# Kernel tuning notes

Measured on AMD Instinct MI355X. Metric: run time of the kernel, lower is better.

Reference implementation:

```python
import jax, jax.numpy as jnp
import numpy as np

BS, V, N, C_IN, C_OUT = 8, 4096, 16, 64, 64


def setup_inputs() -> dict:
    key = jax.random.key(0)
    k1, k2, k3, k4, k5 = jax.random.split(key, 5)
    stdv = 1.0 / np.sqrt(N * C_IN)
    return {
        "neighbor_index": jax.random.randint(k1, (BS, V, N), 0, V, dtype=jnp.int64),
        "vertices": jax.random.normal(k2, (BS, V, 3), dtype=jnp.float32),
        "feature_map": jax.random.normal(k3, (BS, V, C_IN), dtype=jnp.float32),
        "weights": jax.random.uniform(k4, (C_OUT, (N + 1) * C_IN), dtype=jnp.float32, minval=-stdv, maxval=stdv),
        "bias": jax.random.uniform(k5, (C_OUT,), dtype=jnp.float32, minval=-stdv, maxval=stdv),
    }


def reference(neighbor_index, vertices, feature_map, weights, bias):
    bs, v, n = neighbor_index.shape
    # gather neighbor features per batch element: (bs, v, n, c)
    neighbors = jax.vmap(lambda f, idx: f[idx])(feature_map, neighbor_index)
    # prepend self feature: (bs, v, n+1, c)
    feats = jnp.concatenate([feature_map[:, :, None, :], neighbors], axis=2)
    # torch permutes to (bs, c, n+1, v) then reshapes -> flat index = c*(n+1)+k,
    # equivalent to transposing last two dims here before flattening
    flat = feats.transpose(0, 1, 3, 2).reshape(bs, v, -1)  # (bs, v, c*(n+1))
    out = jnp.einsum('bvf,of->bvo', flat, weights) + bias
    return jax.nn.relu(out)
```

## Files before the change

kernel.cpp:

```cpp
#include <hip/hip_runtime.h>
#include <stdint.h>

#define NV 4096

typedef __attribute__((ext_vector_type(8))) short bf16x8;
typedef __attribute__((ext_vector_type(4))) float f32x4;

__device__ __forceinline__ unsigned short f2bf(float f) {
  union { float f; unsigned int u; } v; v.f = f;
  unsigned int r = v.u + 0x7FFF + ((v.u >> 16) & 1);
  return (unsigned short)(r >> 16);
}

__global__ __launch_bounds__(256)
void prep(const float* __restrict__ fm, const float* __restrict__ w,
          unsigned short* __restrict__ fmb, unsigned short* __restrict__ wb) {
  int blk = blockIdx.x;
  if (blk < 1024) {
    int i = (blk * 256 + threadIdx.x) * 8;
    float4 v0 = *(const float4*)(fm + i);
    float4 v1 = *(const float4*)(fm + i + 4);
    ushort4 o0, o1;
    o0.x = f2bf(v0.x); o0.y = f2bf(v0.y); o0.z = f2bf(v0.z); o0.w = f2bf(v0.w);
    o1.x = f2bf(v1.x); o1.y = f2bf(v1.y); o1.z = f2bf(v1.z); o1.w = f2bf(v1.w);
    *(ushort4*)(fmb + i) = o0;
    *(ushort4*)(fmb + i + 4) = o1;
  } else {
    int t = (blk - 1024) * 256 + threadIdx.x;
    int c = t & 63;
    int o = (t >> 6) & 63;
    int k = t >> 12;
    wb[t] = f2bf(w[o * 1088 + c * 17 + k]);
  }
}

__global__ __launch_bounds__(256, 2)
void conv_main(const int* __restrict__ nbr, const unsigned short* __restrict__ fmb,
               const unsigned short* __restrict__ wb, const float* __restrict__ bias,
               float* __restrict__ out) {
  __shared__ unsigned char smem[49152];

  const int bid = blockIdx.x;
  const int b = bid & 7;
  const int tile = bid >> 3;
  const int tid = threadIdx.x;
  const int lane = tid & 63;
  const int lm = lane & 15;
  const int lk = lane >> 4;
  const int w4 = tid >> 6;
  const int rg = w4 >> 1;
  const int h = w4 & 1;

  const int rbase = tile * 64;
  const bf16x8* fb8 = (const bf16x8*)(fmb + (size_t)b * NV * 64);

  const int r0 = tid >> 3;
  const int c8 = tid & 7;
  const int swz = c8 ^ (r0 & 7);
  const int row0g = rbase + r0;
  const int row1g = rbase + r0 + 32;

  const int4* q0 = (const int4*)(nbr + ((size_t)b * NV + row0g) * 16);
  const int4* q1 = (const int4*)(nbr + ((size_t)b * NV + row1g) * 16);
  const int4 i0a = q0[0], i0b = q0[1], i0c = q0[2], i0d = q0[3];
  const int4 i1a = q1[0], i1b = q1[1], i1c = q1[2], i1d = q1[3];

  const int fsl = h * 4 + lk;
  const int offW = lm * 128 + ((fsl ^ (lm & 7)) << 4);
  const int rowL0 = rg * 32 + lm;
  const int rowL1 = rg * 32 + 16 + lm;
  const int offA0 = rowL0 * 128 + ((fsl ^ (rowL0 & 7)) << 4);
  const int offA1 = rowL1 * 128 + ((fsl ^ (rowL1 & 7)) << 4);

  f32x4 accA0{0,0,0,0}, accA1{0,0,0,0}, accA2{0,0,0,0}, accA3{0,0,0,0};
  f32x4 accB0{0,0,0,0}, accB1{0,0,0,0}, accB2{0,0,0,0}, accB3{0,0,0,0};

#define SBR __builtin_amdgcn_sched_barrier(0)
#define MFMA __builtin_amdgcn_mfma_f32_16x16x32_bf16

#define STAGE(SLOT, BUF, SVA, SVB) {                                        \
    _Pragma("unroll")                                                       \
    for (int i_ = 0; i_ < 2; ++i_) {                                        \
      int t_ = i_ * 256 + tid;                                              \
      int o_ = t_ >> 3, s_ = t_ & 7;                                        \
      const unsigned short* ws_ =                                           \
          wb + (SLOT) * 4096 + o_ * 64 + ((s_ ^ (o_ & 7)) << 3);            \
      __builtin_amdgcn_global_load_lds(                                     \
          (const __attribute__((address_space(1))) void*)ws_,               \
          (__attribute__((address_space(3))) void*)(smem + (BUF) * 8192 + t_ * 16), \
          16, 0, 0);                                                        \
    }                                                                       \
    {                                                                       \
      const bf16x8* fa_ = fb8 + (size_t)(SVA) * 8 + swz;                    \
      __builtin_amdgcn_global_load_lds(                                     \
          (const __attribute__((address_space(1))) void*)fa_,               \
          (__attribute__((address_space(3))) void*)(smem + 24576 + (BUF) * 8192 + tid * 16), \
          16, 0, 0);                                                        \
      const bf16x8* fbp_ = fb8 + (size_t)(SVB) * 8 + swz;                   \
      __builtin_amdgcn_global_load_lds(                                     \
          (const __attribute__((address_space(1))) void*)fbp_,              \
          (__attribute__((address_space(3))) void*)(smem + 24576 + (BUF) * 8192 + 4096 + tid * 16), \
          16, 0, 0);                                                        \
    }                                                                       \
  }

#define CONSUME(BUF) {                                                     \
    const char* wp_ = (const char*)smem + (BUF) * 8192;                    \
    const char* fp_ = (const char*)smem + 24576 + (BUF) * 8192;            \
    bf16x8 W0 = *(const bf16x8*)(wp_ + 0 * 2048 + offW);                   \
    bf16x8 W1 = *(const bf16x8*)(wp_ + 1 * 2048 + offW);                   \
    bf16x8 W2 = *(const bf16x8*)(wp_ + 2 * 2048 + offW);                   \
    bf16x8 W3 = *(const bf16x8*)(wp_ + 3 * 2048 + offW);                   \
    bf16x8 A0 = *(const bf16x8*)(fp_ + offA0);                             \
    bf16x8 A1 = *(const bf16x8*)(fp_ + offA1);                             \
    accA0 = MFMA(A0, W0, accA0, 0, 0, 0);                                  \
    accA1 = MFMA(A0, W1, accA1, 0, 0, 0);                                  \
    accA2 = MFMA(A0, W2, accA2, 0, 0, 0);                                  \
    accA3 = MFMA(A0, W3, accA3, 0, 0, 0);                                  \
    accB0 = MFMA(A1, W0, accB0, 0, 0, 0);                                  \
    accB1 = MFMA(A1, W1, accB1, 0, 0, 0);                                  \
    accB2 = MFMA(A1, W2, accB2, 0, 0, 0);                                  \
    accB3 = MFMA(A1, W3, accB3, 0, 0, 0);                                  \
  }

#define WAITBAR(N)                                                          \
    SBR; asm volatile("s_waitcnt vmcnt(" #N ")" ::: "memory"); SBR;         \
    __builtin_amdgcn_s_barrier(); SBR;

  STAGE(0, 0, row0g, row1g); SBR;
  STAGE(1, 1, i0a.x, i1a.x); SBR;
  WAITBAR(4);

  STAGE(2, 2, i0a.y, i1a.y);  SBR; CONSUME(0); WAITBAR(4);
  STAGE(3, 0, i0a.z, i1a.z);  SBR; CONSUME(1); WAITBAR(4);
  STAGE(4, 1, i0a.w, i1a.w);  SBR; CONSUME(2); WAITBAR(4);
  STAGE(5, 2, i0b.x, i1b.x);  SBR; CONSUME(0); WAITBAR(4);
  STAGE(6, 0, i0b.y, i1b.y);  SBR; CONSUME(1); WAITBAR(4);
  STAGE(7, 1, i0b.z, i1b.z);  SBR; CONSUME(2); WAITBAR(4);
  STAGE(8, 2, i0b.w, i1b.w);  SBR; CONSUME(0); WAITBAR(4);
  STAGE(9, 0, i0c.x, i1c.x);  SBR; CONSUME(1); WAITBAR(4);
  STAGE(10, 1, i0c.y, i1c.y); SBR; CONSUME(2); WAITBAR(4);
  STAGE(11, 2, i0c.z, i1c.z); SBR; CONSUME(0); WAITBAR(4);
  STAGE(12, 0, i0c.w, i1c.w); SBR; CONSUME(1); WAITBAR(4);
  STAGE(13, 1, i0d.x, i1d.x); SBR; CONSUME(2); WAITBAR(4);
  STAGE(14, 2, i0d.y, i1d.y); SBR; CONSUME(0); WAITBAR(4);
  STAGE(15, 0, i0d.z, i1d.z); SBR; CONSUME(1); WAITBAR(4);
  STAGE(16, 1, i0d.w, i1d.w); SBR; CONSUME(2); WAITBAR(4);
  CONSUME(0); WAITBAR(0);
  CONSUME(1);

#undef WAITBAR
#undef CONSUME
#undef STAGE
#undef MFMA
#undef SBR

  __syncthreads();
  if (h == 1) {
    float* rp = (float*)smem + rg * 2048 + lane * 4;
    *(f32x4*)(rp + 0 * 256) = accA0;
    *(f32x4*)(rp + 1 * 256) = accA1;
    *(f32x4*)(rp + 2 * 256) = accA2;
    *(f32x4*)(rp + 3 * 256) = accA3;
    *(f32x4*)(rp + 4 * 256) = accB0;
    *(f32x4*)(rp + 5 * 256) = accB1;
    *(f32x4*)(rp + 6 * 256) = accB2;
    *(f32x4*)(rp + 7 * 256) = accB3;
  }
  __syncthreads();
  if (h == 0) {
    const float* rp = (const float*)smem + rg * 2048 + lane * 4;
    accA0 += *(const f32x4*)(rp + 0 * 256);
    accA1 += *(const f32x4*)(rp + 1 * 256);
    accA2 += *(const f32x4*)(rp + 2 * 256);
    accA3 += *(const f32x4*)(rp + 3 * 256);
    accB0 += *(const f32x4*)(rp + 4 * 256);
    accB1 += *(const f32x4*)(rp + 5 * 256);
    accB2 += *(const f32x4*)(rp + 6 * 256);
    accB3 += *(const f32x4*)(rp + 7 * 256);

    const float bv0 = bias[lm];
    const float bv1 = bias[16 + lm];
    const float bv2 = bias[32 + lm];
    const float bv3 = bias[48 + lm];
    float* op = out + (size_t)b * NV * 64;
    #pragma unroll
    for (int mt = 0; mt < 2; ++mt) {
      const int gv = rbase + rg * 32 + mt * 16 + lk * 4;
      #pragma unroll
      for (int r = 0; r < 4; ++r) {
        float* orow = op + (size_t)(gv + r) * 64;
        if (mt == 0) {
          orow[lm]      = fmaxf(accA0[r] + bv0, 0.f);
          orow[16 + lm] = fmaxf(accA1[r] + bv1, 0.f);
          orow[32 + lm] = fmaxf(accA2[r] + bv2, 0.f);
          orow[48 + lm] = fmaxf(accA3[r] + bv3, 0.f);
        } else {
          orow[lm]      = fmaxf(accB0[r] + bv0, 0.f);
          orow[16 + lm] = fmaxf(accB1[r] + bv1, 0.f);
          orow[32 + lm] = fmaxf(accB2[r] + bv2, 0.f);
          orow[48 + lm] = fmaxf(accB3[r] + bv3, 0.f);
        }
      }
    }
  }
}

extern "C" void kernel_launch(void* const* d_in, const int* in_sizes, int n_in,
                              void* d_out, int out_size, void* d_ws, size_t ws_size,
                              hipStream_t stream) {
  const int* nbr = (const int*)d_in[0];
  const float* fm = (const float*)d_in[2];
  const float* w = (const float*)d_in[3];
  const float* bias = (const float*)d_in[4];
  float* out = (float*)d_out;

  unsigned short* fmb = (unsigned short*)d_ws;
  unsigned short* wb = fmb + (size_t)8 * NV * 64;

  prep<<<1296, 256, 0, stream>>>(fm, w, fmb, wb);
  conv_main<<<512, 256, 0, stream>>>(nbr, fmb, wb, bias, out);
}
```

Measured before the change: 19.88 us.

## Preload all weights into LDS and give each wave a private gather pipeline

After: 23.01 us. 1.16x slower.

```diff
diff --git a/kernel.cpp b/kernel.cpp
--- a/kernel.cpp
+++ b/kernel.cpp
@@ -34,11 +34,11 @@
   }
 }
 
-__global__ __launch_bounds__(256, 2)
+__global__ __launch_bounds__(256, 1)
 void conv_main(const int* __restrict__ nbr, const unsigned short* __restrict__ fmb,
                const unsigned short* __restrict__ wb, const float* __restrict__ bias,
                float* __restrict__ out) {
-  __shared__ unsigned char smem[49152];
+  extern __shared__ unsigned char smem[];
 
   const int bid = blockIdx.x;
   const int b = bid & 7;
@@ -54,104 +54,133 @@
   const int rbase = tile * 64;
   const bf16x8* fb8 = (const bf16x8*)(fmb + (size_t)b * NV * 64);
 
-  const int r0 = tid >> 3;
-  const int c8 = tid & 7;
-  const int swz = c8 ^ (r0 & 7);
-  const int row0g = rbase + r0;
-  const int row1g = rbase + r0 + 32;
-
-  const int4* q0 = (const int4*)(nbr + ((size_t)b * NV + row0g) * 16);
-  const int4* q1 = (const int4*)(nbr + ((size_t)b * NV + row1g) * 16);
-  const int4 i0a = q0[0], i0b = q0[1], i0c = q0[2], i0d = q0[3];
-  const int4 i1a = q1[0], i1b = q1[1], i1c = q1[2], i1d = q1[3];
+  const int grA = rbase + rg * 32 + (lane >> 2);
+  const int grB = grA + 16;
+  const int gsrc = h * 4 + ((lane & 3) ^ ((lane >> 3) & 3));
+
+  const int4* qA = (const int4*)(nbr + ((size_t)b * NV + grA) * 16);
+  const int4* qB = (const int4*)(nbr + ((size_t)b * NV + grB) * 16);
+  const int4 iAa = qA[0], iAb = qA[1], iAc = qA[2], iAd = qA[3];
+  const int4 iBa = qB[0], iBb = qB[1], iBc = qB[2], iBd = qB[3];
 
   const int fsl = h * 4 + lk;
+  const bf16x8* w16p = (const bf16x8*)(wb + 16 * 4096);
+  const bf16x8 X0 = w16p[(0 * 16 + lm) * 8 + fsl];
+  const bf16x8 X1 = w16p[(1 * 16 + lm) * 8 + fsl];
+  const bf16x8 X2 = w16p[(2 * 16 + lm) * 8 + fsl];
+  const bf16x8 X3 = w16p[(3 * 16 + lm) * 8 + fsl];
+
+#define SBR __builtin_amdgcn_sched_barrier(0)
+#define MFMA __builtin_amdgcn_mfma_f32_16x16x32_bf16
+
+  #pragma unroll
+  for (int i = 0; i < 32; ++i) {
+    int t = i * 256 + tid;
+    int o = (t >> 3) & 63;
+    int s8 = t & 7;
+    int seg = s8 ^ (o & 7);
+    const unsigned short* src = wb + (size_t)(t >> 9) * 4096 + o * 64 + seg * 8;
+    __builtin_amdgcn_global_load_lds(
+        (const __attribute__((address_space(1))) void*)src,
+        (__attribute__((address_space(3))) void*)(smem + (size_t)t * 16), 16, 0, 0);
+  }
+  SBR;
+
+  unsigned char* fbase = smem + 131072 + w4 * 6144;
+
+#define STAGE_F(SA, SB, C) {                                                 \
+    const bf16x8* sa_ = fb8 + (size_t)(SA) * 8 + gsrc;                       \
+    __builtin_amdgcn_global_load_lds(                                        \
+        (const __attribute__((address_space(1))) void*)sa_,                  \
+        (__attribute__((address_space(3))) void*)(fbase + (C) * 2048 + lane * 16), \
+        16, 0, 0);                                                           \
+    const bf16x8* sb_ = fb8 + (size_t)(SB) * 8 + gsrc;                       \
+    __builtin_amdgcn_global_load_lds(                                        \
+        (const __attribute__((address_space(1))) void*)sb_,                  \
+        (__attribute__((address_space(3))) void*)(fbase + (C) * 2048 + 1024 + lane * 16), \
+        16, 0, 0);                                                           \
+  }
+
+  STAGE_F(grA, grB, 0); SBR;
+  STAGE_F(iAa.x, iBa.x, 1); SBR;
+  STAGE_F(iAa.y, iBa.y, 2); SBR;
+  asm volatile("s_waitcnt vmcnt(6)" ::: "memory"); SBR;
+  __syncthreads();
+
+  const int offA0 = lm * 64 + ((lk ^ ((lm >> 1) & 3)) << 4);
   const int offW = lm * 128 + ((fsl ^ (lm & 7)) << 4);
-  const int rowL0 = rg * 32 + lm;
-  const int rowL1 = rg * 32 + 16 + lm;
-  const int offA0 = rowL0 * 128 + ((fsl ^ (rowL0 & 7)) << 4);
-  const int offA1 = rowL1 * 128 + ((fsl ^ (rowL1 & 7)) << 4);
 
   f32x4 accA0{0,0,0,0}, accA1{0,0,0,0}, accA2{0,0,0,0}, accA3{0,0,0,0};
   f32x4 accB0{0,0,0,0}, accB1{0,0,0,0}, accB2{0,0,0,0}, accB3{0,0,0,0};
 
-#define SBR __builtin_amdgcn_sched_barrier(0)
-#define MFMA __builtin_amdgcn_mfma_f32_16x16x32_bf16
-
-#define STAGE(SLOT, BUF, SVA, SVB) {                                        \
-    _Pragma("unroll")                                                       \
-    for (int i_ = 0; i_ < 2; ++i_) {                                        \
-      int t_ = i_ * 256 + tid;                                              \
-      int o_ = t_ >> 3, s_ = t_ & 7;                                        \
-      const unsigned short* ws_ =                                           \
-          wb + (SLOT) * 4096 + o_ * 64 + ((s_ ^ (o_ & 7)) << 3);            \
-      __builtin_amdgcn_global_load_lds(                                     \
-          (const __attribute__((address_space(1))) void*)ws_,               \
-          (__attribute__((address_space(3))) void*)(smem + (BUF) * 8192 + t_ * 16), \
-          16, 0, 0);                                                        \
-    }                                                                       \
-    {                                                                       \
-      const bf16x8* fa_ = fb8 + (size_t)(SVA) * 8 + swz;                    \
-      __builtin_amdgcn_global_load_lds(                                     \
-          (const __attribute__((address_space(1))) void*)fa_,               \
-          (__attribute__((address_space(3))) void*)(smem + 24576 + (BUF) * 8192 + tid * 16), \
-          16, 0, 0);                                                        \
-      const bf16x8* fbp_ = fb8 + (size_t)(SVB) * 8 + swz;                   \
-      __builtin_amdgcn_global_load_lds(                                     \
-          (const __attribute__((address_space(1))) void*)fbp_,              \
-          (__attribute__((address_space(3))) void*)(smem + 24576 + (BUF) * 8192 + 4096 + tid * 16), \
-          16, 0, 0);                                                        \
-    }                                                                       \
-  }
-
-#define CONSUME(BUF) {                                                     \
-    const char* wp_ = (const char*)smem + (BUF) * 8192;                    \
-    const char* fp_ = (const char*)smem + 24576 + (BUF) * 8192;            \
-    bf16x8 W0 = *(const bf16x8*)(wp_ + 0 * 2048 + offW);                   \
-    bf16x8 W1 = *(const bf16x8*)(wp_ + 1 * 2048 + offW);                   \
-    bf16x8 W2 = *(const bf16x8*)(wp_ + 2 * 2048 + offW);                   \
-    bf16x8 W3 = *(const bf16x8*)(wp_ + 3 * 2048 + offW);                   \
-    bf16x8 A0 = *(const bf16x8*)(fp_ + offA0);                             \
-    bf16x8 A1 = *(const bf16x8*)(fp_ + offA1);                             \
-    accA0 = MFMA(A0, W0, accA0, 0, 0, 0);                                  \
-    accA1 = MFMA(A0, W1, accA1, 0, 0, 0);                                  \
-    accA2 = MFMA(A0, W2, accA2, 0, 0, 0);                                  \
-    accA3 = MFMA(A0, W3, accA3, 0, 0, 0);                                  \
-    accB0 = MFMA(A1, W0, accB0, 0, 0, 0);                                  \
-    accB1 = MFMA(A1, W1, accB1, 0, 0, 0);                                  \
-    accB2 = MFMA(A1, W2, accB2, 0, 0, 0);                                  \
-    accB3 = MFMA(A1, W3, accB3, 0, 0, 0);                                  \
-  }
-
-#define WAITBAR(N)                                                          \
-    SBR; asm volatile("s_waitcnt vmcnt(" #N ")" ::: "memory"); SBR;         \
-    __builtin_amdgcn_s_barrier(); SBR;
-
-  STAGE(0, 0, row0g, row1g); SBR;
-  STAGE(1, 1, i0a.x, i1a.x); SBR;
-  WAITBAR(4);
-
-  STAGE(2, 2, i0a.y, i1a.y);  SBR; CONSUME(0); WAITBAR(4);
-  STAGE(3, 0, i0a.z, i1a.z);  SBR; CONSUME(1); WAITBAR(4);
-  STAGE(4, 1, i0a.w, i1a.w);  SBR; CONSUME(2); WAITBAR(4);
-  STAGE(5, 2, i0b.x, i1b.x);  SBR; CONSUME(0); WAITBAR(4);
-  STAGE(6, 0, i0b.y, i1b.y);  SBR; CONSUME(1); WAITBAR(4);
-  STAGE(7, 1, i0b.z, i1b.z);  SBR; CONSUME(2); WAITBAR(4);
-  STAGE(8, 2, i0b.w, i1b.w);  SBR; CONSUME(0); WAITBAR(4);
-  STAGE(9, 0, i0c.x, i1c.x);  SBR; CONSUME(1); WAITBAR(4);
-  STAGE(10, 1, i0c.y, i1c.y); SBR; CONSUME(2); WAITBAR(4);
-  STAGE(11, 2, i0c.z, i1c.z); SBR; CONSUME(0); WAITBAR(4);
-  STAGE(12, 0, i0c.w, i1c.w); SBR; CONSUME(1); WAITBAR(4);
-  STAGE(13, 1, i0d.x, i1d.x); SBR; CONSUME(2); WAITBAR(4);
-  STAGE(14, 2, i0d.y, i1d.y); SBR; CONSUME(0); WAITBAR(4);
-  STAGE(15, 0, i0d.z, i1d.z); SBR; CONSUME(1); WAITBAR(4);
-  STAGE(16, 1, i0d.w, i1d.w); SBR; CONSUME(2); WAITBAR(4);
-  CONSUME(0); WAITBAR(0);
-  CONSUME(1);
-
-#undef WAITBAR
-#undef CONSUME
-#undef STAGE
+#define MFMAS(W0_, W1_, W2_, W3_)                                  \
+    accA0 = MFMA(A0, W0_, accA0, 0, 0, 0);                         \
+    accA1 = MFMA(A0, W1_, accA1, 0, 0, 0);                         \
+    accA2 = MFMA(A0, W2_, accA2, 0, 0, 0);                         \
+    accA3 = MFMA(A0, W3_, accA3, 0, 0, 0);                         \
+    accB0 = MFMA(A1, W0_, accB0, 0, 0, 0);                         \
+    accB1 = MFMA(A1, W1_, accB1, 0, 0, 0);                         \
+    accB2 = MFMA(A1, W2_, accB2, 0, 0, 0);                         \
+    accB3 = MFMA(A1, W3_, accB3, 0, 0, 0);
+
+#define STEP(K, CNT, SAN, SBN)                                               \
+  asm volatile("s_waitcnt vmcnt(" #CNT ")" ::: "memory"); SBR;               \
+  {                                                                          \
+    const unsigned char* fp_ = fbase + ((K) % 3) * 2048;                     \
+    bf16x8 A0 = *(const bf16x8*)(fp_ + offA0);                               \
+    bf16x8 A1 = *(const bf16x8*)(fp_ + 1024 + offA0);                        \
+    const unsigned char* wp_ = smem + (K) * 8192;                            \
+    bf16x8 W0 = *(const bf16x8*)(wp_ + offW);                                \
+    bf16x8 W1 = *(const bf16x8*)(wp_ + 2048 + offW);                         \
+    bf16x8 W2 = *(const bf16x8*)(wp_ + 4096 + offW);                         \
+    bf16x8 W3 = *(const bf16x8*)(wp_ + 6144 + offW);                         \
+    asm volatile("s_waitcnt lgkmcnt(0)" ::: "memory"); SBR;                  \
+    STAGE_F(SAN, SBN, (K) % 3); SBR;                                         \
+    MFMAS(W0, W1, W2, W3)                                                    \
+  }
+
+#define STEPN(K, CNT)                                                        \
+  asm volatile("s_waitcnt vmcnt(" #CNT ")" ::: "memory"); SBR;               \
+  {                                                                          \
+    const unsigned char* fp_ = fbase + ((K) % 3) * 2048;                     \
+    bf16x8 A0 = *(const bf16x8*)(fp_ + offA0);                               \
+    bf16x8 A1 = *(const bf16x8*)(fp_ + 1024 + offA0);                        \
+    const unsigned char* wp_ = smem + (K) * 8192;                            \
+    bf16x8 W0 = *(const bf16x8*)(wp_ + offW);                                \
+    bf16x8 W1 = *(const bf16x8*)(wp_ + 2048 + offW);                         \
+    bf16x8 W2 = *(const bf16x8*)(wp_ + 4096 + offW);                         \
+    bf16x8 W3 = *(const bf16x8*)(wp_ + 6144 + offW);                         \
+    MFMAS(W0, W1, W2, W3)                                                    \
+  }
+
+  STEP(0, 4, iAa.z, iBa.z)
+  STEP(1, 4, iAa.w, iBa.w)
+  STEP(2, 4, iAb.x, iBb.x)
+  STEP(3, 4, iAb.y, iBb.y)
+  STEP(4, 4, iAb.z, iBb.z)
+  STEP(5, 4, iAb.w, iBb.w)
+  STEP(6, 4, iAc.x, iBc.x)
+  STEP(7, 4, iAc.y, iBc.y)
+  STEP(8, 4, iAc.z, iBc.z)
+  STEP(9, 4, iAc.w, iBc.w)
+  STEP(10, 4, iAd.x, iBd.x)
+  STEP(11, 4, iAd.y, iBd.y)
+  STEP(12, 4, iAd.z, iBd.z)
+  STEP(13, 4, iAd.w, iBd.w)
+  STEPN(14, 4)
+  STEPN(15, 2)
+  asm volatile("s_waitcnt vmcnt(0)" ::: "memory"); SBR;
+  {
+    const unsigned char* fp_ = fbase + 1 * 2048;
+    bf16x8 A0 = *(const bf16x8*)(fp_ + offA0);
+    bf16x8 A1 = *(const bf16x8*)(fp_ + 1024 + offA0);
+    MFMAS(X0, X1, X2, X3)
+  }
+
+#undef STEPN
+#undef STEP
+#undef MFMAS
+#undef STAGE_F
 #undef MFMA
 #undef SBR
 
@@ -218,6 +247,9 @@
   unsigned short* fmb = (unsigned short*)d_ws;
   unsigned short* wb = fmb + (size_t)8 * NV * 64;
 
+  hipFuncSetAttribute((const void*)conv_main,
+                      hipFuncAttributeMaxDynamicSharedMemorySize, 155648);
+
   prep<<<1296, 256, 0, stream>>>(fm, w, fmb, wb);
-  conv_main<<<512, 256, 0, stream>>>(nbr, fmb, wb, bias, out);
-}
+  conv_main<<<512, 256, 155648, stream>>>(nbr, fmb, wb, bias, out);
+}
```

## Gather fp32 features directly and convert to bf16 in the main kernel

Applied to the files above, without the earlier changes.

Result: slower. 21.99 us (+10.6%).

```diff
diff --git a/kernel.cpp b/kernel.cpp
--- a/kernel.cpp
+++ b/kernel.cpp
@@ -1,4 +1,5 @@
 #include <hip/hip_runtime.h>
+#include <hip/hip_bf16.h>
 #include <stdint.h>
 
 #define NV 4096
@@ -13,32 +14,28 @@
 }
 
 __global__ __launch_bounds__(256)
-void prep(const float* __restrict__ fm, const float* __restrict__ w,
-          unsigned short* __restrict__ fmb, unsigned short* __restrict__ wb) {
-  int blk = blockIdx.x;
-  if (blk < 1024) {
-    int i = (blk * 256 + threadIdx.x) * 8;
-    float4 v0 = *(const float4*)(fm + i);
-    float4 v1 = *(const float4*)(fm + i + 4);
-    ushort4 o0, o1;
-    o0.x = f2bf(v0.x); o0.y = f2bf(v0.y); o0.z = f2bf(v0.z); o0.w = f2bf(v0.w);
-    o1.x = f2bf(v1.x); o1.y = f2bf(v1.y); o1.z = f2bf(v1.z); o1.w = f2bf(v1.w);
-    *(ushort4*)(fmb + i) = o0;
-    *(ushort4*)(fmb + i + 4) = o1;
-  } else {
-    int t = (blk - 1024) * 256 + threadIdx.x;
-    int c = t & 63;
-    int o = (t >> 6) & 63;
-    int k = t >> 12;
-    wb[t] = f2bf(w[o * 1088 + c * 17 + k]);
-  }
+void prep_w(const float* __restrict__ w, unsigned short* __restrict__ wb) {
+  int t = blockIdx.x * 256 + threadIdx.x;
+  int c = t & 63;
+  int o = (t >> 6) & 63;
+  int k = t >> 12;
+  wb[t] = f2bf(w[o * 1088 + c * 17 + k]);
+}
+
+__device__ __forceinline__ bf16x8 cvt8(f32x4 lo, f32x4 hi) {
+  union { bf16x8 v; __hip_bfloat162 h[4]; } u;
+  u.h[0] = __float22bfloat162_rn(make_float2(lo[0], lo[1]));
+  u.h[1] = __float22bfloat162_rn(make_float2(lo[2], lo[3]));
+  u.h[2] = __float22bfloat162_rn(make_float2(hi[0], hi[1]));
+  u.h[3] = __float22bfloat162_rn(make_float2(hi[2], hi[3]));
+  return u.v;
 }
 
 __global__ __launch_bounds__(256, 2)
-void conv_main(const int* __restrict__ nbr, const unsigned short* __restrict__ fmb,
+void conv_main(const int* __restrict__ nbr, const float* __restrict__ fm,
                const unsigned short* __restrict__ wb, const float* __restrict__ bias,
                float* __restrict__ out) {
-  __shared__ unsigned char smem[49152];
+  __shared__ unsigned char smem[77824];
 
   const int bid = blockIdx.x;
   const int b = bid & 7;
@@ -52,25 +49,11 @@
   const int h = w4 & 1;
 
   const int rbase = tile * 64;
-  const bf16x8* fb8 = (const bf16x8*)(fmb + (size_t)b * NV * 64);
-
-  const int r0 = tid >> 3;
-  const int c8 = tid & 7;
-  const int swz = c8 ^ (r0 & 7);
-  const int row0g = rbase + r0;
-  const int row1g = rbase + r0 + 32;
-
-  const int4* q0 = (const int4*)(nbr + ((size_t)b * NV + row0g) * 16);
-  const int4* q1 = (const int4*)(nbr + ((size_t)b * NV + row1g) * 16);
-  const int4 i0a = q0[0], i0b = q0[1], i0c = q0[2], i0d = q0[3];
-  const int4 i1a = q1[0], i1b = q1[1], i1c = q1[2], i1d = q1[3];
+  const float* fb32 = fm + (size_t)b * NV * 64;
 
   const int fsl = h * 4 + lk;
   const int offW = lm * 128 + ((fsl ^ (lm & 7)) << 4);
-  const int rowL0 = rg * 32 + lm;
-  const int rowL1 = rg * 32 + 16 + lm;
-  const int offA0 = rowL0 * 128 + ((fsl ^ (rowL0 & 7)) << 4);
-  const int offA1 = rowL1 * 128 + ((fsl ^ (rowL1 & 7)) << 4);
+  const int offF0 = (rg * 32 + lm) * 256 + (((2 * fsl) ^ ((lm & 7) << 1)) << 4);
 
   f32x4 accA0{0,0,0,0}, accA1{0,0,0,0}, accA2{0,0,0,0}, accA3{0,0,0,0};
   f32x4 accB0{0,0,0,0}, accB1{0,0,0,0}, accB2{0,0,0,0}, accB3{0,0,0,0};
@@ -78,41 +61,47 @@
 #define SBR __builtin_amdgcn_sched_barrier(0)
 #define MFMA __builtin_amdgcn_mfma_f32_16x16x32_bf16
 
-#define STAGE(SLOT, BUF, SVA, SVB) {                                        \
+#define STAGE(K, C) {                                                       \
     _Pragma("unroll")                                                       \
     for (int i_ = 0; i_ < 2; ++i_) {                                        \
       int t_ = i_ * 256 + tid;                                              \
-      int o_ = t_ >> 3, s_ = t_ & 7;                                        \
+      int o_ = (t_ >> 3) & 63, s_ = t_ & 7;                                 \
       const unsigned short* ws_ =                                           \
-          wb + (SLOT) * 4096 + o_ * 64 + ((s_ ^ (o_ & 7)) << 3);            \
+          wb + (K) * 4096 + o_ * 64 + ((s_ ^ (o_ & 7)) << 3);               \
       __builtin_amdgcn_global_load_lds(                                     \
           (const __attribute__((address_space(1))) void*)ws_,               \
-          (__attribute__((address_space(3))) void*)(smem + (BUF) * 8192 + t_ * 16), \
+          (__attribute__((address_space(3))) void*)(smem + (C) * 8192 + t_ * 16), \
           16, 0, 0);                                                        \
     }                                                                       \
-    {                                                                       \
-      const bf16x8* fa_ = fb8 + (size_t)(SVA) * 8 + swz;                    \
+    _Pragma("unroll")                                                       \
+    for (int i_ = 0; i_ < 4; ++i_) {                                        \
+      int row_ = w4 * 16 + i_ * 4 + (lane >> 4);                            \
+      int sv_;                                                              \
+      if ((K) == 0) sv_ = rbase + row_;                                     \
+      else sv_ = *(const int*)(smem + 73728 + row_ * 64 + ((K) - 1) * 4);   \
+      int gs_ = (lane & 15) ^ ((row_ & 7) << 1);                            \
+      const float* fs_ = fb32 + (size_t)sv_ * 64 + gs_ * 4;                 \
       __builtin_amdgcn_global_load_lds(                                     \
-          (const __attribute__((address_space(1))) void*)fa_,               \
-          (__attribute__((address_space(3))) void*)(smem + 24576 + (BUF) * 8192 + tid * 16), \
-          16, 0, 0);                                                        \
-      const bf16x8* fbp_ = fb8 + (size_t)(SVB) * 8 + swz;                   \
-      __builtin_amdgcn_global_load_lds(                                     \
-          (const __attribute__((address_space(1))) void*)fbp_,              \
-          (__attribute__((address_space(3))) void*)(smem + 24576 + (BUF) * 8192 + 4096 + tid * 16), \
+          (const __attribute__((address_space(1))) void*)fs_,               \
+          (__attribute__((address_space(3))) void*)(smem + 24576 + (C) * 16384 \
+              + (size_t)row_ * 256 + (lane & 15) * 16),                     \
           16, 0, 0);                                                        \
     }                                                                       \
   }
 
-#define CONSUME(BUF) {                                                     \
-    const char* wp_ = (const char*)smem + (BUF) * 8192;                    \
-    const char* fp_ = (const char*)smem + 24576 + (BUF) * 8192;            \
+#define CONSUME(K, C) {                                                    \
+    const unsigned char* wp_ = smem + (C) * 8192;                          \
+    const unsigned char* fp_ = smem + 24576 + (C) * 16384;                 \
     bf16x8 W0 = *(const bf16x8*)(wp_ + 0 * 2048 + offW);                   \
     bf16x8 W1 = *(const bf16x8*)(wp_ + 1 * 2048 + offW);                   \
     bf16x8 W2 = *(const bf16x8*)(wp_ + 2 * 2048 + offW);                   \
     bf16x8 W3 = *(const bf16x8*)(wp_ + 3 * 2048 + offW);                   \
-    bf16x8 A0 = *(const bf16x8*)(fp_ + offA0);                             \
-    bf16x8 A1 = *(const bf16x8*)(fp_ + offA1);                             \
+    f32x4 lo0 = *(const f32x4*)(fp_ + offF0);                              \
+    f32x4 hi0 = *(const f32x4*)(fp_ + offF0 + 16);                         \
+    f32x4 lo1 = *(const f32x4*)(fp_ + offF0 + 4096);                       \
+    f32x4 hi1 = *(const f32x4*)(fp_ + offF0 + 4096 + 16);                  \
+    bf16x8 A0 = cvt8(lo0, hi0);                                            \
+    bf16x8 A1 = cvt8(lo1, hi1);                                            \
     accA0 = MFMA(A0, W0, accA0, 0, 0, 0);                                  \
     accA1 = MFMA(A0, W1, accA1, 0, 0, 0);                                  \
     accA2 = MFMA(A0, W2, accA2, 0, 0, 0);                                  \
@@ -127,27 +116,29 @@
     SBR; asm volatile("s_waitcnt vmcnt(" #N ")" ::: "memory"); SBR;         \
     __builtin_amdgcn_s_barrier(); SBR;
 
-  STAGE(0, 0, row0g, row1g); SBR;
-  STAGE(1, 1, i0a.x, i1a.x); SBR;
-  WAITBAR(4);
-
-  STAGE(2, 2, i0a.y, i1a.y);  SBR; CONSUME(0); WAITBAR(4);
-  STAGE(3, 0, i0a.z, i1a.z);  SBR; CONSUME(1); WAITBAR(4);
-  STAGE(4, 1, i0a.w, i1a.w);  SBR; CONSUME(2); WAITBAR(4);
-  STAGE(5, 2, i0b.x, i1b.x);  SBR; CONSUME(0); WAITBAR(4);
-  STAGE(6, 0, i0b.y, i1b.y);  SBR; CONSUME(1); WAITBAR(4);
-  STAGE(7, 1, i0b.z, i1b.z);  SBR; CONSUME(2); WAITBAR(4);
-  STAGE(8, 2, i0b.w, i1b.w);  SBR; CONSUME(0); WAITBAR(4);
-  STAGE(9, 0, i0c.x, i1c.x);  SBR; CONSUME(1); WAITBAR(4);
-  STAGE(10, 1, i0c.y, i1c.y); SBR; CONSUME(2); WAITBAR(4);
-  STAGE(11, 2, i0c.z, i1c.z); SBR; CONSUME(0); WAITBAR(4);
-  STAGE(12, 0, i0c.w, i1c.w); SBR; CONSUME(1); WAITBAR(4);
-  STAGE(13, 1, i0d.x, i1d.x); SBR; CONSUME(2); WAITBAR(4);
-  STAGE(14, 2, i0d.y, i1d.y); SBR; CONSUME(0); WAITBAR(4);
-  STAGE(15, 0, i0d.z, i1d.z); SBR; CONSUME(1); WAITBAR(4);
-  STAGE(16, 1, i0d.w, i1d.w); SBR; CONSUME(2); WAITBAR(4);
-  CONSUME(0); WAITBAR(0);
-  CONSUME(1);
+  const int4 myidx = ((const int4*)(nbr + ((size_t)b * NV + rbase) * 16))[tid];
+  STAGE(0, 0); SBR;
+  ((int4*)(smem + 73728))[tid] = myidx;
+  __syncthreads();
+  STAGE(1, 1); SBR;
+
+  STAGE(2, 2);  SBR; CONSUME(0, 0);  WAITBAR(6);
+  STAGE(3, 0);  SBR; CONSUME(1, 1);  WAITBAR(6);
+  STAGE(4, 1);  SBR; CONSUME(2, 2);  WAITBAR(6);
+  STAGE(5, 2);  SBR; CONSUME(3, 0);  WAITBAR(6);
+  STAGE(6, 0);  SBR; CONSUME(4, 1);  WAITBAR(6);
+  STAGE(7, 1);  SBR; CONSUME(5, 2);  WAITBAR(6);
+  STAGE(8, 2);  SBR; CONSUME(6, 0);  WAITBAR(6);
+  STAGE(9, 0);  SBR; CONSUME(7, 1);  WAITBAR(6);
+  STAGE(10, 1); SBR; CONSUME(8, 2);  WAITBAR(6);
+  STAGE(11, 2); SBR; CONSUME(9, 0);  WAITBAR(6);
+  STAGE(12, 0); SBR; CONSUME(10, 1); WAITBAR(6);
+  STAGE(13, 1); SBR; CONSUME(11, 2); WAITBAR(6);
+  STAGE(14, 2); SBR; CONSUME(12, 0); WAITBAR(6);
+  STAGE(15, 0); SBR; CONSUME(13, 1); WAITBAR(6);
+  STAGE(16, 1); SBR; CONSUME(14, 2); WAITBAR(6);
+  CONSUME(15, 0); WAITBAR(0);
+  CONSUME(16, 1);
 
 #undef WAITBAR
 #undef CONSUME
@@ -215,9 +206,8 @@
   const float* bias = (const float*)d_in[4];
   float* out = (float*)d_out;
 
-  unsigned short* fmb = (unsigned short*)d_ws;
-  unsigned short* wb = fmb + (size_t)8 * NV * 64;
-
-  prep<<<1296, 256, 0, stream>>>(fm, w, fmb, wb);
-  conv_main<<<512, 256, 0, stream>>>(nbr, fmb, wb, bias, out);
-}
+  unsigned short* wb = (unsigned short*)d_ws;
+
+  prep_w<<<272, 256, 0, stream>>>(w, wb);
+  conv_main<<<512, 256, 0, stream>>>(nbr, fm, wb, bias, out);
+}
```

## Split K across four waves with full 64x64 tiles and cross-wave LDS reduction

Applied to the files above, without the earlier changes.

Result: slower. 20.64 us (+3.8%).

```diff
diff --git a/kernel.cpp b/kernel.cpp
--- a/kernel.cpp
+++ b/kernel.cpp
@@ -48,8 +48,8 @@
   const int lm = lane & 15;
   const int lk = lane >> 4;
   const int w4 = tid >> 6;
-  const int rg = w4 >> 1;
-  const int h = w4 & 1;
+  const int p = w4 & 1;
+  const int h = w4 >> 1;
 
   const int rbase = tile * 64;
   const bf16x8* fb8 = (const bf16x8*)(fmb + (size_t)b * NV * 64);
@@ -66,23 +66,21 @@
   const int4 i1a = q1[0], i1b = q1[1], i1c = q1[2], i1d = q1[3];
 
   const int fsl = h * 4 + lk;
-  const int offW = lm * 128 + ((fsl ^ (lm & 7)) << 4);
-  const int rowL0 = rg * 32 + lm;
-  const int rowL1 = rg * 32 + 16 + lm;
-  const int offA0 = rowL0 * 128 + ((fsl ^ (rowL0 & 7)) << 4);
-  const int offA1 = rowL1 * 128 + ((fsl ^ (rowL1 & 7)) << 4);
-
-  f32x4 accA0{0,0,0,0}, accA1{0,0,0,0}, accA2{0,0,0,0}, accA3{0,0,0,0};
-  f32x4 accB0{0,0,0,0}, accB1{0,0,0,0}, accB2{0,0,0,0}, accB3{0,0,0,0};
+  const int offB = lm * 128 + ((fsl ^ (lm & 7)) << 4);
+
+  f32x4 acc00{0,0,0,0}, acc01{0,0,0,0}, acc02{0,0,0,0}, acc03{0,0,0,0};
+  f32x4 acc10{0,0,0,0}, acc11{0,0,0,0}, acc12{0,0,0,0}, acc13{0,0,0,0};
+  f32x4 acc20{0,0,0,0}, acc21{0,0,0,0}, acc22{0,0,0,0}, acc23{0,0,0,0};
+  f32x4 acc30{0,0,0,0}, acc31{0,0,0,0}, acc32{0,0,0,0}, acc33{0,0,0,0};
 
 #define SBR __builtin_amdgcn_sched_barrier(0)
 #define MFMA __builtin_amdgcn_mfma_f32_16x16x32_bf16
 
-#define STAGE(SLOT, BUF, SVA, SVB) {                                        \
+#define STAGE(SLOT, BUF) {                                                  \
     _Pragma("unroll")                                                       \
     for (int i_ = 0; i_ < 2; ++i_) {                                        \
       int t_ = i_ * 256 + tid;                                              \
-      int o_ = t_ >> 3, s_ = t_ & 7;                                        \
+      int o_ = (t_ >> 3) & 63, s_ = t_ & 7;                                 \
       const unsigned short* ws_ =                                           \
           wb + (SLOT) * 4096 + o_ * 64 + ((s_ ^ (o_ & 7)) << 3);            \
       __builtin_amdgcn_global_load_lds(                                     \
@@ -91,119 +89,116 @@
           16, 0, 0);                                                        \
     }                                                                       \
     {                                                                       \
-      const bf16x8* fa_ = fb8 + (size_t)(SVA) * 8 + swz;                    \
+      const bf16x8* fa_ = fb8 + (size_t)(SVA_) * 8 + swz;                   \
       __builtin_amdgcn_global_load_lds(                                     \
           (const __attribute__((address_space(1))) void*)fa_,               \
           (__attribute__((address_space(3))) void*)(smem + 24576 + (BUF) * 8192 + tid * 16), \
           16, 0, 0);                                                        \
-      const bf16x8* fbp_ = fb8 + (size_t)(SVB) * 8 + swz;                   \
+      const bf16x8* fbp_ = fb8 + (size_t)(SVB_) * 8 + swz;                  \
       __builtin_amdgcn_global_load_lds(                                     \
           (const __attribute__((address_space(1))) void*)fbp_,              \
           (__attribute__((address_space(3))) void*)(smem + 24576 + (BUF) * 8192 + 4096 + tid * 16), \
           16, 0, 0);                                                        \
     }                                                                       \
   }
+#define STAGES(SLOT, BUF, SA, SB) { const int SVA_ = (SA), SVB_ = (SB); STAGE(SLOT, BUF) }
 
 #define CONSUME(BUF) {                                                     \
-    const char* wp_ = (const char*)smem + (BUF) * 8192;                    \
-    const char* fp_ = (const char*)smem + 24576 + (BUF) * 8192;            \
-    bf16x8 W0 = *(const bf16x8*)(wp_ + 0 * 2048 + offW);                   \
-    bf16x8 W1 = *(const bf16x8*)(wp_ + 1 * 2048 + offW);                   \
-    bf16x8 W2 = *(const bf16x8*)(wp_ + 2 * 2048 + offW);                   \
-    bf16x8 W3 = *(const bf16x8*)(wp_ + 3 * 2048 + offW);                   \
-    bf16x8 A0 = *(const bf16x8*)(fp_ + offA0);                             \
-    bf16x8 A1 = *(const bf16x8*)(fp_ + offA1);                             \
-    accA0 = MFMA(A0, W0, accA0, 0, 0, 0);                                  \
-    accA1 = MFMA(A0, W1, accA1, 0, 0, 0);                                  \
-    accA2 = MFMA(A0, W2, accA2, 0, 0, 0);                                  \
-    accA3 = MFMA(A0, W3, accA3, 0, 0, 0);                                  \
-    accB0 = MFMA(A1, W0, accB0, 0, 0, 0);                                  \
-    accB1 = MFMA(A1, W1, accB1, 0, 0, 0);                                  \
-    accB2 = MFMA(A1, W2, accB2, 0, 0, 0);                                  \
-    accB3 = MFMA(A1, W3, accB3, 0, 0, 0);                                  \
+    const unsigned char* wp_ = smem + (BUF) * 8192;                        \
+    const unsigned char* fp_ = smem + 24576 + (BUF) * 8192;                \
+    bf16x8 W0 = *(const bf16x8*)(wp_ + offB);                              \
+    bf16x8 W1 = *(const bf16x8*)(wp_ + 2048 + offB);                       \
+    bf16x8 W2 = *(const bf16x8*)(wp_ + 4096 + offB);                       \
+    bf16x8 W3 = *(const bf16x8*)(wp_ + 6144 + offB);                       \
+    bf16x8 A0 = *(const bf16x8*)(fp_ + offB);                              \
+    bf16x8 A1 = *(const bf16x8*)(fp_ + 2048 + offB);                       \
+    bf16x8 A2 = *(const bf16x8*)(fp_ + 4096 + offB);                       \
+    bf16x8 A3 = *(const bf16x8*)(fp_ + 6144 + offB);                       \
+    __builtin_amdgcn_s_setprio(1);                                         \
+    acc00 = MFMA(A0, W0, acc00, 0, 0, 0);                                  \
+    acc01 = MFMA(A0, W1, acc01, 0, 0, 0);                                  \
+    acc02 = MFMA(A0, W2, acc02, 0, 0, 0);                                  \
+    acc03 = MFMA(A0, W3, acc03, 0, 0, 0);                                  \
+    acc10 = MFMA(A1, W0, acc10, 0, 0, 0);                                  \
+    acc11 = MFMA(A1, W1, acc11, 0, 0, 0);                                  \
+    acc12 = MFMA(A1, W2, acc12, 0, 0, 0);                                  \
+    acc13 = MFMA(A1, W3, acc13, 0, 0, 0);                                  \
+    acc20 = MFMA(A2, W0, acc20, 0, 0, 0);                                  \
+    acc21 = MFMA(A2, W1, acc21, 0, 0, 0);                                  \
+    acc22 = MFMA(A2, W2, acc22, 0, 0, 0);                                  \
+    acc23 = MFMA(A2, W3, acc23, 0, 0, 0);                                  \
+    acc30 = MFMA(A3, W0, acc30, 0, 0, 0);                                  \
+    acc31 = MFMA(A3, W1, acc31, 0, 0, 0);                                  \
+    acc32 = MFMA(A3, W2, acc32, 0, 0, 0);                                  \
+    acc33 = MFMA(A3, W3, acc33, 0, 0, 0);                                  \
+    __builtin_amdgcn_s_setprio(0);                                         \
   }
 
 #define WAITBAR(N)                                                          \
     SBR; asm volatile("s_waitcnt vmcnt(" #N ")" ::: "memory"); SBR;         \
     __builtin_amdgcn_s_barrier(); SBR;
 
-  STAGE(0, 0, row0g, row1g); SBR;
-  STAGE(1, 1, i0a.x, i1a.x); SBR;
+  STAGES(0, 0, row0g, row1g); SBR;
+  STAGES(1, 1, i0a.x, i1a.x); SBR;
   WAITBAR(4);
 
-  STAGE(2, 2, i0a.y, i1a.y);  SBR; CONSUME(0); WAITBAR(4);
-  STAGE(3, 0, i0a.z, i1a.z);  SBR; CONSUME(1); WAITBAR(4);
-  STAGE(4, 1, i0a.w, i1a.w);  SBR; CONSUME(2); WAITBAR(4);
-  STAGE(5, 2, i0b.x, i1b.x);  SBR; CONSUME(0); WAITBAR(4);
-  STAGE(6, 0, i0b.y, i1b.y);  SBR; CONSUME(1); WAITBAR(4);
-  STAGE(7, 1, i0b.z, i1b.z);  SBR; CONSUME(2); WAITBAR(4);
-  STAGE(8, 2, i0b.w, i1b.w);  SBR; CONSUME(0); WAITBAR(4);
-  STAGE(9, 0, i0c.x, i1c.x);  SBR; CONSUME(1); WAITBAR(4);
-  STAGE(10, 1, i0c.y, i1c.y); SBR; CONSUME(2); WAITBAR(4);
-  STAGE(11, 2, i0c.z, i1c.z); SBR; CONSUME(0); WAITBAR(4);
-  STAGE(12, 0, i0c.w, i1c.w); SBR; CONSUME(1); WAITBAR(4);
-  STAGE(13, 1, i0d.x, i1d.x); SBR; CONSUME(2); WAITBAR(4);
-  STAGE(14, 2, i0d.y, i1d.y); SBR; CONSUME(0); WAITBAR(4);
-  STAGE(15, 0, i0d.z, i1d.z); SBR; CONSUME(1); WAITBAR(4);
-  STAGE(16, 1, i0d.w, i1d.w); SBR; CONSUME(2); WAITBAR(4);
-  CONSUME(0); WAITBAR(0);
-  CONSUME(1);
+  STAGES(2, 2, i0a.y, i1a.y);  SBR; if (p == 0) CONSUME(0); WAITBAR(4);
+  STAGES(3, 0, i0a.z, i1a.z);  SBR; if (p == 1) CONSUME(1); WAITBAR(4);
+  STAGES(4, 1, i0a.w, i1a.w);  SBR; if (p == 0) CONSUME(2); WAITBAR(4);
+  STAGES(5, 2, i0b.x, i1b.x);  SBR; if (p == 1) CONSUME(0); WAITBAR(4);
+  STAGES(6, 0, i0b.y, i1b.y);  SBR; if (p == 0) CONSUME(1); WAITBAR(4);
+  STAGES(7, 1, i0b.z, i1b.z);  SBR; if (p == 1) CONSUME(2); WAITBAR(4);
+  STAGES(8, 2, i0b.w, i1b.w);  SBR; if (p == 0) CONSUME(0); WAITBAR(4);
+  STAGES(9, 0, i0c.x, i1c.x);  SBR; if (p == 1) CONSUME(1); WAITBAR(4);
+  STAGES(10, 1, i0c.y, i1c.y); SBR; if (p == 0) CONSUME(2); WAITBAR(4);
+  STAGES(11, 2, i0c.z, i1c.z); SBR; if (p == 1) CONSUME(0); WAITBAR(4);
+  STAGES(12, 0, i0c.w, i1c.w); SBR; if (p == 0) CONSUME(1); WAITBAR(4);
+  STAGES(13, 1, i0d.x, i1d.x); SBR; if (p == 1) CONSUME(2); WAITBAR(4);
+  STAGES(14, 2, i0d.y, i1d.y); SBR; if (p == 0) CONSUME(0); WAITBAR(4);
+  STAGES(15, 0, i0d.z, i1d.z); SBR; if (p == 1) CONSUME(1); WAITBAR(4);
+  STAGES(16, 1, i0d.w, i1d.w); SBR; if (p == 0) CONSUME(2); WAITBAR(4);
+  if (p == 1) CONSUME(0); WAITBAR(0);
+  if (p == 0) CONSUME(1);
 
 #undef WAITBAR
 #undef CONSUME
+#undef STAGES
 #undef STAGE
 #undef MFMA
 #undef SBR
 
-  __syncthreads();
-  if (h == 1) {
-    float* rp = (float*)smem + rg * 2048 + lane * 4;
-    *(f32x4*)(rp + 0 * 256) = accA0;
-    *(f32x4*)(rp + 1 * 256) = accA1;
-    *(f32x4*)(rp + 2 * 256) = accA2;
-    *(f32x4*)(rp + 3 * 256) = accA3;
-    *(f32x4*)(rp + 4 * 256) = accB0;
-    *(f32x4*)(rp + 5 * 256) = accB1;
-    *(f32x4*)(rp + 6 * 256) = accB2;
-    *(f32x4*)(rp + 7 * 256) = accB3;
-  }
-  __syncthreads();
-  if (h == 0) {
-    const float* rp = (const float*)smem + rg * 2048 + lane * 4;
-    accA0 += *(const f32x4*)(rp + 0 * 256);
-    accA1 += *(const f32x4*)(rp + 1 * 256);
-    accA2 += *(const f32x4*)(rp + 2 * 256);
-    accA3 += *(const f32x4*)(rp + 3 * 256);
-    accB0 += *(const f32x4*)(rp + 4 * 256);
-    accB1 += *(const f32x4*)(rp + 5 * 256);
-    accB2 += *(const f32x4*)(rp + 6 * 256);
-    accB3 += *(const f32x4*)(rp + 7 * 256);
-
-    const float bv0 = bias[lm];
-    const float bv1 = bias[16 + lm];
-    const float bv2 = bias[32 + lm];
-    const float bv3 = bias[48 + lm];
-    float* op = out + (size_t)b * NV * 64;
-    #pragma unroll
-    for (int mt = 0; mt < 2; ++mt) {
-      const int gv = rbase + rg * 32 + mt * 16 + lk * 4;
-      #pragma unroll
-      for (int r = 0; r < 4; ++r) {
-        float* orow = op + (size_t)(gv + r) * 64;
-        if (mt == 0) {
-          orow[lm]      = fmaxf(accA0[r] + bv0, 0.f);
-          orow[16 + lm] = fmaxf(accA1[r] + bv1, 0.f);
-          orow[32 + lm] = fmaxf(accA2[r] + bv2, 0.f);
-          orow[48 + lm] = fmaxf(accA3[r] + bv3, 0.f);
-        } else {
-          orow[lm]      = fmaxf(accB0[r] + bv0, 0.f);
-          orow[16 + lm] = fmaxf(accB1[r] + bv1, 0.f);
-          orow[32 + lm] = fmaxf(accB2[r] + bv2, 0.f);
-          orow[48 + lm] = fmaxf(accB3[r] + bv3, 0.f);
-        }
-      }
-    }
-  }
+  float* op = out + (size_t)b * NV * 64;
+#define REDROUND(RTB, a0x0, a0x1, a0x2, a0x3, a1x0, a1x1, a1x2, a1x3)       \
+  __syncthreads();                                                          \
+  {                                                                         \
+    unsigned char* wr_ = smem + w4 * 8192 + lane * 16;                      \
+    *(f32x4*)(wr_ + 0 * 1024) = a0x0; *(f32x4*)(wr_ + 1 * 1024) = a0x1;     \
+    *(f32x4*)(wr_ + 2 * 1024) = a0x2; *(f32x4*)(wr_ + 3 * 1024) = a0x3;     \
+    *(f32x4*)(wr_ + 4 * 1024) = a1x0; *(f32x4*)(wr_ + 5 * 1024) = a1x1;     \
+    *(f32x4*)(wr_ + 6 * 1024) = a1x2; *(f32x4*)(wr_ + 7 * 1024) = a1x3;     \
+  }                                                                         \
+  __syncthreads();                                                          \
+  _Pragma("unroll")                                                         \
+  for (int j_ = 0; j_ < 2; ++j_) {                                          \
+    int cell_ = w4 * 2 + j_;                                                \
+    const unsigned char* rb_ = smem + cell_ * 1024 + lane * 16;             \
+    f32x4 s_ = *(const f32x4*)(rb_);                                        \
+    s_ += *(const f32x4*)(rb_ + 8192);                                      \
+    s_ += *(const f32x4*)(rb_ + 16384);                                     \
+    s_ += *(const f32x4*)(rb_ + 24576);                                     \
+    int rt_ = (RTB) + (cell_ >> 2);                                         \
+    int n_ = cell_ & 3;                                                     \
+    int o_ = n_ * 16 + lm;                                                  \
+    float bv_ = bias[o_];                                                   \
+    int gv_ = rbase + rt_ * 16 + lk * 4;                                    \
+    _Pragma("unroll")                                                       \
+    for (int r_ = 0; r_ < 4; ++r_)                                          \
+      op[(size_t)(gv_ + r_) * 64 + o_] = fmaxf(s_[r_] + bv_, 0.f);          \
+  }
+
+  REDROUND(0, acc00, acc01, acc02, acc03, acc10, acc11, acc12, acc13)
+  REDROUND(2, acc20, acc21, acc22, acc23, acc30, acc31, acc32, acc33)
+#undef REDROUND
 }
 
 extern "C" void kernel_launch(void* const* d_in, const int* in_sizes, int n_in,
```
